# Kernel optimization log

Hardware: AMD Instinct MI355X
Metric: run time of the kernel (lower is better)

## Reference

```python
import jax, jax.numpy as jnp
import numpy as np

HEADS = 8
NEG_SLOPE = 0.2


def _gat_conv(x, src, dst, W, a_src, a_dst, b, heads, ch):
    # PyG GATConv (v1), eval mode (dropout inactive), add_self_loops=True, concat=True.
    N = x.shape[0]
    loop = jnp.arange(N)
    s = jnp.concatenate([src, loop])
    d = jnp.concatenate([dst, loop])
    h = (x @ W).reshape(N, heads, ch)                      # [N, H, C]
    alpha_src = jnp.einsum('nhc,hc->nh', h, a_src)          # [N, H]
    alpha_dst = jnp.einsum('nhc,hc->nh', h, a_dst)
    e = jax.nn.leaky_relu(alpha_src[s] + alpha_dst[d], NEG_SLOPE)  # [E, H]
    m = jax.ops.segment_max(e, d, num_segments=N)           # segment softmax over dst
    ex = jnp.exp(e - m[d])
    denom = jax.ops.segment_sum(ex, d, num_segments=N)
    alpha = ex / (denom[d] + 1e-16)
    out = jax.ops.segment_sum(h[s] * alpha[:, :, None], d, num_segments=N)  # [N, H, C]
    return out.reshape(N, heads * ch) + b


def setup_inputs() -> dict:
    key = jax.random.key(0)
    ks = jax.random.split(key, 20)
    B, N, F_in = 8, 1024, 16
    E = 131072
    C1, C2 = 8, 128                     # per-head channels of conv1 / conv2
    D = N * HEADS * C2                  # flattened head input = 1024*1024
    NA, AC = 4, 4                       # len(num_actions)=4, each 4 actions

    def w(k, shape, fan_in):
        return jax.random.normal(k, shape, jnp.float32) * (1.0 / np.sqrt(fan_in))

    inp = {
        'x': jax.random.normal(ks[0], (B, N, F_in), jnp.float32),
        'edge': jax.random.randint(ks[1], (2, E), 0, B * N, jnp.int64),
        'W1': w(ks[2], (F_in, HEADS * C1), F_in),
        'a_src1': w(ks[3], (HEADS, C1), C1),
        'a_dst1': w(ks[4], (HEADS, C1), C1),
        'b1': jnp.zeros((HEADS * C1,), jnp.float32),
        'W2': w(ks[5], (HEADS * C1, HEADS * C2), HEADS * C1),
        'a_src2': w(ks[6], (HEADS, C2), C2),
        'a_dst2': w(ks[7], (HEADS, C2), C2),
        'b2': jnp.zeros((HEADS * C2,), jnp.float32),
        'adv_w': w(ks[8], (D, NA * AC), D),
        'adv_b': jnp.zeros((NA * AC,), jnp.float32),
        'val1_w': w(ks[9], (D, 64), D),
        'val1_b': jnp.zeros((64,), jnp.float32),
        'val2_w': w(ks[10], (64, 64), 64),
        'val2_b': jnp.zeros((64,), jnp.float32),
        'val3_w': w(ks[11], (64, 1), 64),
        'val3_b': jnp.zeros((1,), jnp.float32),
    }
    return inp


def reference(x, edge, W1, a_src1, a_dst1, b1, W2, a_src2, a_dst2, b2,
              adv_w, adv_b, val1_w, val1_b, val2_w, val2_b, val3_w, val3_b):
    B, N, F_in = x.shape
    src, dst = edge[0], edge[1]
    h = x.reshape(B * N, F_in)
    h = jax.nn.relu(_gat_conv(h, src, dst, W1, a_src1, a_dst1, b1, HEADS, 8))
    h = jax.nn.relu(_gat_conv(h, src, dst, W2, a_src2, a_dst2, b2, HEADS, 128))
    h = h.reshape(B, -1)                                   # [B, N*1024]
    adv = jax.nn.relu(h @ adv_w + adv_b).reshape(B, 4, 4)  # [B, len(num_actions), actions]
    v = jax.nn.relu(h @ val1_w + val1_b)
    v = jax.nn.relu(v @ val2_w + val2_b)
    v = v @ val3_w + val3_b                                # [B, 1]
    return v[:, :, None] + adv - adv.mean(-1, keepdims=True)
```

## Files before the change

### kernel.cpp

```cpp
#include <hip/hip_runtime.h>
#include <stdint.h>

#define NODES   8192
#define BATCH   8
#define FIN     16
#define HC1     64
#define HC2     1024
#define DTOT    1048576
#define NEG     0.2f

typedef unsigned short u16;

__device__ __forceinline__ float b2f(u16 s){ return __uint_as_float(((unsigned)s)<<16); }
__device__ __forceinline__ u16 f2b(float f){
    unsigned u = __float_as_uint(f);
    unsigned r = u + 0x7fffu + ((u>>16)&1u);
    return (u16)(r>>16);
}
__device__ __forceinline__ float lrelu(float x){ return x > 0.f ? x : NEG*x; }
__device__ __forceinline__ float ldf(const void* p, long i, int isf){
    return isf ? ((const float*)p)[i] : b2f(((const u16*)p)[i]);
}

__global__ void k_detect(const u16* __restrict__ xs, const int* __restrict__ ed, int* flags){
    __shared__ int cnt[2];
    int t = threadIdx.x;
    if(t<2) cnt[t]=0;
    __syncthreads();
    int bad=0;
    for(int i=t;i<1024;i+=256){
        u16 u = xs[i];
        float a = fabsf(b2f(u));
        if(!(u==0 || (a>1e-8f && a<1e4f))) bad++;
    }
    if(bad) atomicAdd(&cnt[0], bad);
    int z=0;
    for(int i=t;i<1024;i+=256){
        if(ed[2*i+1]==0) z++;
    }
    if(z) atomicAdd(&cnt[1], z);
    __syncthreads();
    if(t==0){ flags[0] = (cnt[0] > 64) ? 1 : 0; flags[1] = (cnt[1] > 512) ? 1 : 0; }
}

__device__ __forceinline__ int esrc(const int* e, int i, int i64){ return i64 ? e[2*i] : e[i]; }
__device__ __forceinline__ int edst(const int* e, int i, int E, int i64){ return i64 ? e[2*(E+i)] : e[E+i]; }

__global__ void k_zero(int* counts){
    int i = blockIdx.x*256 + threadIdx.x;
    if(i < NODES) counts[i] = 0;
}

__global__ void k_count(const int* __restrict__ ed, int E, int* counts, const int* flags){
    int i64 = flags[1];
    int e = blockIdx.x*256 + threadIdx.x;
    if(e < E) atomicAdd(&counts[edst(ed,e,E,i64)], 1);
}

__global__ __launch_bounds__(1024) void k_scan(const int* __restrict__ counts, int* offs, int* cursor){
    __shared__ int sums[1024];
    int t = threadIdx.x;
    int base = t*8;
    int loc[8]; int s = 0;
    for(int k=0;k<8;k++){ loc[k] = s; s += counts[base+k]; }
    sums[t] = s;
    __syncthreads();
    for(int off=1; off<1024; off<<=1){
        int v = (t>=off) ? sums[t-off] : 0;
        __syncthreads();
        sums[t] += v;
        __syncthreads();
    }
    int b = (t==0) ? 0 : sums[t-1];
    for(int k=0;k<8;k++){ int v = b + loc[k]; offs[base+k]=v; cursor[base+k]=v; }
    if(t==1023) offs[NODES] = sums[1023];
}

__global__ void k_fill(const int* __restrict__ ed, int E, int* cursor, int* csr, const int* flags){
    int i64 = flags[1];
    int e = blockIdx.x*256 + threadIdx.x;
    if(e < E){ int p = atomicAdd(&cursor[edst(ed,e,E,i64)], 1); csr[p] = esrc(ed,e,i64); }
}

__global__ __launch_bounds__(256) void k_dense1(const void* __restrict__ x,
        const void* __restrict__ W1, const void* __restrict__ asw, const void* __restrict__ adw,
        float* g1, float* as1, float* ad1, const int* flags){
    int isf = flags[0];
    __shared__ float w1[FIN*HC1];
    __shared__ float av[64], dv[64];
    __shared__ float xr[4][FIN];
    __shared__ float hrow[4][HC1];
    int t = threadIdx.x;
    int n0 = blockIdx.x*4;
    for(int i=t;i<FIN*HC1;i+=256) w1[i] = ldf(W1,i,isf);
    if(t<64){ av[t]=ldf(asw,t,isf); dv[t]=ldf(adw,t,isf); }
    if(t<64) xr[t>>4][t&15] = ldf(x, n0*FIN + t, isf);
    __syncthreads();
    int i = t>>6, c = t&63;
    float acc = 0.f;
    #pragma unroll
    for(int k=0;k<FIN;k++) acc += xr[i][k]*w1[k*HC1+c];
    g1[(n0+i)*HC1 + c] = acc;
    hrow[i][c] = acc;
    __syncthreads();
    if(t<32){
        int ii=t>>3, h=t&7;
        float sa=0.f, sd=0.f;
        #pragma unroll
        for(int k=0;k<8;k++){ float v=hrow[ii][h*8+k]; sa+=v*av[h*8+k]; sd+=v*dv[h*8+k]; }
        as1[(n0+ii)*8+h]=sa; ad1[(n0+ii)*8+h]=sd;
    }
}

__global__ __launch_bounds__(64) void k_agg1(const int* __restrict__ offs, const int* __restrict__ csr,
        const float* __restrict__ g1, const float* __restrict__ as1, const float* __restrict__ ad1,
        const void* __restrict__ b1, float* z1, const int* flags){
    int isf = flags[0];
    __shared__ float redm[64], redd[64];
    __shared__ float mh[8], dh[8], adl[8];
    __shared__ int src_l[64];
    __shared__ float wx[64*8];
    int n = blockIdx.x, t = threadIdx.x;
    int off = offs[n], deg = offs[n+1]-off, tot = deg+1;
    if(t<8) adl[t] = ad1[n*8+t];
    __syncthreads();
    {
        int h = t&7, jg = t>>3;
        float ad = adl[h];
        float m = -1e30f, d = 0.f;
        for(int j=jg; j<tot; j+=8){
            int s = (j<deg)?csr[off+j]:n;
            float e = lrelu(as1[s*8+h] + ad);
            if(e>m){ d = d*__expf(m-e) + 1.f; m = e; } else d += __expf(e-m);
        }
        redm[t]=m; redd[t]=d;
        __syncthreads();
        for(int st=4; st>=1; st>>=1){
            if(jg < st){
                float m2 = redm[t + st*8], d2 = redd[t + st*8];
                float mm = fmaxf(m, m2);
                d = d*__expf(m-mm) + d2*__expf(m2-mm);
                m = mm;
                redm[t]=m; redd[t]=d;
            }
            __syncthreads();
        }
        if(t<8){ mh[t]=redm[t]; dh[t]=redd[t] + 1e-16f; }
        __syncthreads();
    }
    int c = t, hc = t>>3;
    float acc = 0.f;
    for(int c0=0;c0<tot;c0+=64){
        int nc = min(64, tot-c0);
        if(t<nc){ int j=c0+t; src_l[t]=(j<deg)?csr[off+j]:n; }
        __syncthreads();
        for(int p=t;p<nc*8;p+=64){
            int j=p>>3, hh=p&7;
            float e = lrelu(as1[src_l[j]*8+hh] + adl[hh]);
            wx[p] = __expf(e - mh[hh]);
        }
        __syncthreads();
        for(int j=0;j<nc;j++) acc += wx[j*8+hc]*g1[src_l[j]*HC1 + c];
        __syncthreads();
    }
    z1[n*HC1 + c] = fmaxf(acc/dh[hc] + ldf(b1,c,isf), 0.f);
}

__global__ __launch_bounds__(256) void k_dense2(const float* __restrict__ z1,
        const void* __restrict__ W2, u16* g2, const int* flags){
    int isf = flags[0];
    __shared__ float zr[8][HC1];
    int t = threadIdx.x;
    int n0 = blockIdx.x*8;
    for(int i=t;i<8*HC1;i+=256) zr[i>>6][i&63] = z1[n0*HC1 + i];
    __syncthreads();
    int c0 = t*4;
    float acc[8][4];
    #pragma unroll
    for(int i=0;i<8;i++){ acc[i][0]=0;acc[i][1]=0;acc[i][2]=0;acc[i][3]=0; }
    for(int k=0;k<HC1;k++){
        float w0,w1,w2,w3;
        if(isf){
            float4 w = *(const float4*)((const float*)W2 + (size_t)k*HC2 + c0);
            w0=w.x; w1=w.y; w2=w.z; w3=w.w;
        } else {
            ushort4 w = *(const ushort4*)((const u16*)W2 + (size_t)k*HC2 + c0);
            w0=b2f(w.x); w1=b2f(w.y); w2=b2f(w.z); w3=b2f(w.w);
        }
        #pragma unroll
        for(int i=0;i<8;i++){
            float zv = zr[i][k];
            acc[i][0]+=zv*w0; acc[i][1]+=zv*w1; acc[i][2]+=zv*w2; acc[i][3]+=zv*w3;
        }
    }
    #pragma unroll
    for(int i=0;i<8;i++){
        ushort4 o;
        o.x=f2b(acc[i][0]); o.y=f2b(acc[i][1]); o.z=f2b(acc[i][2]); o.w=f2b(acc[i][3]);
        *(ushort4*)&g2[(size_t)(n0+i)*HC2 + c0] = o;
    }
}

__global__ __launch_bounds__(256) void k_alpha2(const u16* __restrict__ g2,
        const void* __restrict__ asw, const void* __restrict__ adw,
        float* as2, float* ad2, const int* flags){
    int isf = flags[0];
    int n = blockIdx.x, t = threadIdx.x;
    int h = t>>5, l = t&31;
    int c = h*128 + l*4;
    ushort4 gv = *(const ushort4*)&g2[(size_t)n*HC2 + c];
    float s0,s1,s2,s3,d0,d1,d2,d3;
    if(isf){
        float4 sv = *(const float4*)((const float*)asw + c);
        float4 dv = *(const float4*)((const float*)adw + c);
        s0=sv.x;s1=sv.y;s2=sv.z;s3=sv.w; d0=dv.x;d1=dv.y;d2=dv.z;d3=dv.w;
    } else {
        ushort4 sv = *(const ushort4*)((const u16*)asw + c);
        ushort4 dv = *(const ushort4*)((const u16*)adw + c);
        s0=b2f(sv.x);s1=b2f(sv.y);s2=b2f(sv.z);s3=b2f(sv.w);
        d0=b2f(dv.x);d1=b2f(dv.y);d2=b2f(dv.z);d3=b2f(dv.w);
    }
    float g0=b2f(gv.x), g1v=b2f(gv.y), g2v=b2f(gv.z), g3=b2f(gv.w);
    float sa = g0*s0+g1v*s1+g2v*s2+g3*s3;
    float sd = g0*d0+g1v*d1+g2v*d2+g3*d3;
    for(int m=1;m<32;m<<=1){ sa += __shfl_xor(sa,m); sd += __shfl_xor(sd,m); }
    if(l==0){ as2[n*8+h]=sa; ad2[n*8+h]=sd; }
}

__global__ __launch_bounds__(256) void k_agg2(const int* __restrict__ offs, const int* __restrict__ csr,
        const u16* __restrict__ g2, const float* __restrict__ as2, const float* __restrict__ ad2,
        const void* __restrict__ b2, u16* hbf, const int* flags){
    int isf = flags[0];
    __shared__ float redm[256], redd[256];
    __shared__ float mh[8], dh[8], adl[8];
    __shared__ int src_l[64];
    __shared__ float wx[64*8];
    int n = blockIdx.x, t = threadIdx.x;
    int off = offs[n], deg = offs[n+1]-off, tot = deg+1;
    if(t<8) adl[t] = ad2[n*8+t];
    __syncthreads();
    {
        int h = t&7, jg = t>>3;
        float ad = adl[h];
        float m = -1e30f, d = 0.f;
        for(int j=jg; j<tot; j+=32){
            int s = (j<deg)?csr[off+j]:n;
            float e = lrelu(as2[s*8+h] + ad);
            if(e>m){ d = d*__expf(m-e) + 1.f; m = e; } else d += __expf(e-m);
        }
        redm[t]=m; redd[t]=d;
        __syncthreads();
        for(int st=16; st>=1; st>>=1){
            if(jg < st){
                float m2 = redm[t + st*8], d2 = redd[t + st*8];
                float mm = fmaxf(m, m2);
                d = d*__expf(m-mm) + d2*__expf(m2-mm);
                m = mm;
                redm[t]=m; redd[t]=d;
            }
            __syncthreads();
        }
        if(t<8){ mh[t]=redm[t]; dh[t]=redd[t] + 1e-16f; }
        __syncthreads();
    }
    int c0 = t*4, hc = t>>5;
    float acc[4] = {0,0,0,0};
    for(int cc0=0;cc0<tot;cc0+=64){
        int nc = min(64, tot-cc0);
        if(t<nc){ int j=cc0+t; src_l[t]=(j<deg)?csr[off+j]:n; }
        __syncthreads();
        for(int p=t;p<nc*8;p+=256){
            int j=p>>3, hh=p&7;
            float e = lrelu(as2[src_l[j]*8+hh] + adl[hh]);
            wx[p] = __expf(e - mh[hh]);
        }
        __syncthreads();
        for(int j=0;j<nc;j++){
            float w = wx[j*8+hc];
            ushort4 gv = *(const ushort4*)&g2[(size_t)src_l[j]*HC2 + c0];
            acc[0]+=w*b2f(gv.x); acc[1]+=w*b2f(gv.y); acc[2]+=w*b2f(gv.z); acc[3]+=w*b2f(gv.w);
        }
        __syncthreads();
    }
    float dhv = dh[hc];
    ushort4 o;
    o.x = f2b(fmaxf(acc[0]/dhv + ldf(b2,c0+0,isf), 0.f));
    o.y = f2b(fmaxf(acc[1]/dhv + ldf(b2,c0+1,isf), 0.f));
    o.z = f2b(fmaxf(acc[2]/dhv + ldf(b2,c0+2,isf), 0.f));
    o.w = f2b(fmaxf(acc[3]/dhv + ldf(b2,c0+3,isf), 0.f));
    *(ushort4*)&hbf[(size_t)n*HC2 + c0] = o;
}

template<int COLS, int NW>
__device__ __forceinline__ void gemv_part(const void* __restrict__ W, const u16* __restrict__ hbf,
        float* __restrict__ scratch, int wid, int lane, int isf){
    const int GR    = COLS/8;
    const int KSTEP = 64/GR;
    const int ITERS = DTOT/(NW*KSTEP);
    int cg  = (lane % GR)*8;
    int kof = lane / GR;
    float acc[8][8];
    #pragma unroll
    for(int b=0;b<8;b++)
        #pragma unroll
        for(int c=0;c<8;c++) acc[b][c]=0.f;
    for(int it=0; it<ITERS; it++){
        int k = (it*NW + wid)*KSTEP + kof;
        float wv[8];
        if(isf){
            float4 wa = *(const float4*)((const float*)W + (size_t)k*COLS + cg);
            float4 wb = *(const float4*)((const float*)W + (size_t)k*COLS + cg + 4);
            wv[0]=wa.x;wv[1]=wa.y;wv[2]=wa.z;wv[3]=wa.w;
            wv[4]=wb.x;wv[5]=wb.y;wv[6]=wb.z;wv[7]=wb.w;
        } else {
            ushort4 wa = *(const ushort4*)((const u16*)W + (size_t)k*COLS + cg);
            ushort4 wb = *(const ushort4*)((const u16*)W + (size_t)k*COLS + cg + 4);
            wv[0]=b2f(wa.x);wv[1]=b2f(wa.y);wv[2]=b2f(wa.z);wv[3]=b2f(wa.w);
            wv[4]=b2f(wb.x);wv[5]=b2f(wb.y);wv[6]=b2f(wb.z);wv[7]=b2f(wb.w);
        }
        float hv[8];
        #pragma unroll
        for(int b=0;b<8;b++) hv[b] = b2f(hbf[(size_t)b*DTOT + k]);
        #pragma unroll
        for(int b=0;b<8;b++)
            #pragma unroll
            for(int c=0;c<8;c++) acc[b][c] += hv[b]*wv[c];
    }
    #pragma unroll
    for(int m=GR;m<64;m<<=1){
        #pragma unroll
        for(int b=0;b<8;b++)
            #pragma unroll
            for(int c=0;c<8;c++) acc[b][c] += __shfl_xor(acc[b][c], m);
    }
    int q = lane / GR;
    if(q < 8){
        float4 o0, o1;
        o0.x=acc[q][0]; o0.y=acc[q][1]; o0.z=acc[q][2]; o0.w=acc[q][3];
        o1.x=acc[q][4]; o1.y=acc[q][5]; o1.z=acc[q][6]; o1.w=acc[q][7];
        float* dst = scratch + (size_t)wid*COLS*8 + q*COLS + cg;
        *(float4*)dst       = o0;
        *(float4*)(dst + 4) = o1;
    }
}

__global__ __launch_bounds__(256) void k_heads(const void* __restrict__ v1w, const void* __restrict__ advw,
        const u16* __restrict__ hbf, float* s1, float* s2, const int* flags){
    int isf = flags[0];
    int lane = threadIdx.x & 63;
    if(blockIdx.x < 512){
        int wid = (int)((blockIdx.x*256 + threadIdx.x) >> 6);
        gemv_part<64,2048>(v1w, hbf, s1, wid, lane, isf);
    } else {
        int wid = (int)(((blockIdx.x-512)*256 + threadIdx.x) >> 6);
        gemv_part<16,512>(advw, hbf, s2, wid, lane, isf);
    }
}

__global__ __launch_bounds__(256) void k_reduce(const float* __restrict__ s1, const float* __restrict__ s2,
        float* v1a, float* adva){
    __shared__ float red[256];
    int blk = blockIdx.x, t = threadIdx.x;
    if(blk < 8){
        int o = blk*64 + (t&63);
        float a = 0.f;
        for(int p = (t>>6); p < 2048; p += 4) a += s1[(size_t)p*512 + o];
        red[t] = a; __syncthreads();
        if(t<64) v1a[o] = red[t]+red[t+64]+red[t+128]+red[t+192];
    } else {
        int o = (blk-8)*64 + (t&63);
        float a = 0.f;
        for(int p = (t>>6); p < 512; p += 4) a += s2[(size_t)p*128 + o];
        red[t] = a; __syncthreads();
        if(t<64) adva[o] = red[t]+red[t+64]+red[t+128]+red[t+192];
    }
}

__global__ __launch_bounds__(512) void k_final(const float* __restrict__ v1a, const float* __restrict__ adva,
        const void* __restrict__ v1b, const void* __restrict__ advb,
        const void* __restrict__ w2v, const void* __restrict__ b2v,
        const void* __restrict__ w3v, const void* __restrict__ b3v,
        void* out, const int* flags){
    int isf = flags[0];
    __shared__ float v1[8][64], v2[8][64], adv[128], v3[8];
    int t = threadIdx.x;
    { int b=t>>6, j=t&63; v1[b][j] = fmaxf(v1a[t] + ldf(v1b,j,isf), 0.f); }
    if(t<128) adv[t] = fmaxf(adva[t] + ldf(advb,t&15,isf), 0.f);
    __syncthreads();
    { int b=t>>6, j=t&63;
      float a=0.f;
      for(int k=0;k<64;k++) a += v1[b][k]*ldf(w2v,k*64+j,isf);
      v2[b][j] = fmaxf(a + ldf(b2v,j,isf), 0.f); }
    __syncthreads();
    if(t<8){
        float a=0.f;
        for(int k=0;k<64;k++) a += v2[t][k]*ldf(w3v,k,isf);
        v3[t] = a + ldf(b3v,0,isf);
    }
    __syncthreads();
    if(t<128){
        int b=t>>4, r=(t>>2)&3;
        int base = b*16 + r*4;
        float m = 0.25f*(adv[base]+adv[base+1]+adv[base+2]+adv[base+3]);
        float val = v3[b] + adv[t] - m;
        if(isf) ((float*)out)[t] = val;
        else    ((u16*)out)[t]   = f2b(val);
    }
}

extern "C" void kernel_launch(void* const* d_in, const int* in_sizes, int n_in,
                              void* d_out, int out_size, void* d_ws, size_t ws_size,
                              hipStream_t stream){
    const void* x    = d_in[0];
    const int*  edge = (const int*)d_in[1];
    const int E = in_sizes[1]/2;
    const void* W1   = d_in[2];
    const void* as1w = d_in[3];
    const void* ad1w = d_in[4];
    const void* b1   = d_in[5];
    const void* W2   = d_in[6];
    const void* as2w = d_in[7];
    const void* ad2w = d_in[8];
    const void* b2   = d_in[9];
    const void* advw = d_in[10];
    const void* advb = d_in[11];
    const void* v1w  = d_in[12];
    const void* v1b  = d_in[13];
    const void* v2w  = d_in[14];
    const void* v2b  = d_in[15];
    const void* v3w  = d_in[16];
    const void* v3b  = d_in[17];

    char* wsp = (char*)d_ws;
    size_t o = 0;
    auto alloc = [&](size_t bytes)->char*{
        char* p = wsp + o;
        o = (o + bytes + 255) & ~(size_t)255;
        return p;
    };
    int*   flags  = (int*)  alloc(256);
    int*   counts = (int*)  alloc(NODES*4);
    int*   offs   = (int*)  alloc((NODES+8)*4);
    int*   cursor = (int*)  alloc(NODES*4);
    int*   csr    = (int*)  alloc((size_t)E*4);
    float* g1     = (float*)alloc((size_t)NODES*HC1*4);
    float* as1    = (float*)alloc((size_t)NODES*8*4);
    float* ad1    = (float*)alloc((size_t)NODES*8*4);
    float* z1     = (float*)alloc((size_t)NODES*HC1*4);
    u16*   g2     = (u16*)  alloc((size_t)NODES*HC2*2);
    float* as2    = (float*)alloc((size_t)NODES*8*4);
    float* ad2    = (float*)alloc((size_t)NODES*8*4);
    u16*   hbf    = (u16*)  alloc((size_t)NODES*HC2*2);
    float* s1     = (float*)alloc((size_t)2048*512*4);
    float* s2     = (float*)alloc((size_t)512*128*4);
    float* v1a    = (float*)alloc(512*4);
    float* adva   = (float*)alloc(128*4);

    k_detect<<<1, 256, 0, stream>>>((const u16*)x, edge, flags);
    k_zero  <<<32, 256, 0, stream>>>(counts);
    k_count <<<(E+255)/256, 256, 0, stream>>>(edge, E, counts, flags);
    k_scan  <<<1, 1024, 0, stream>>>(counts, offs, cursor);
    k_fill  <<<(E+255)/256, 256, 0, stream>>>(edge, E, cursor, csr, flags);
    k_dense1<<<NODES/4, 256, 0, stream>>>(x, W1, as1w, ad1w, g1, as1, ad1, flags);
    k_agg1  <<<NODES, 64, 0, stream>>>(offs, csr, g1, as1, ad1, b1, z1, flags);
    k_dense2<<<NODES/8, 256, 0, stream>>>(z1, W2, g2, flags);
    k_alpha2<<<NODES, 256, 0, stream>>>(g2, as2w, ad2w, as2, ad2, flags);
    k_agg2  <<<NODES, 256, 0, stream>>>(offs, csr, g2, as2, ad2, b2, hbf, flags);
    k_heads <<<640, 256, 0, stream>>>(v1w, advw, hbf, s1, s2, flags);
    k_reduce<<<10, 256, 0, stream>>>(s1, s2, v1a, adva);
    k_final <<<1, 512, 0, stream>>>(v1a, adva, v1b, advb, v2w, v2b, v3w, v3b, d_out, flags);
}
```

Baseline: 720.6 us.

## Fuse prep/count/dense1 and dense2/alpha2 kernels, unroll gathers, widen head GEMV grid

Merges flag detection with counter zeroing, edge counting with the first dense layer, and the second dense layer with its attention-logit computation, cutting kernel launches and a full re-read of g2. The neighbor-gather loops in both aggregation kernels are unrolled by two to expose more memory-level parallelism. The head GEMV doubles its block count with two k-steps per iteration, and the partial-sum reduction moves to 1024-thread blocks. The larger partial buffers add reduction traffic, and the alpha2 logits are now computed from fp32 accumulators instead of bf16-rounded values, which slightly changes numerics.

```diff
diff --git a/kernel.cpp b/kernel.cpp
--- a/kernel.cpp
+++ b/kernel.cpp
@@ -22,39 +22,71 @@
     return isf ? ((const float*)p)[i] : b2f(((const u16*)p)[i]);
 }
 
-__global__ void k_detect(const u16* __restrict__ xs, const int* __restrict__ ed, int* flags){
-    __shared__ int cnt[2];
-    int t = threadIdx.x;
-    if(t<2) cnt[t]=0;
-    __syncthreads();
-    int bad=0;
-    for(int i=t;i<1024;i+=256){
-        u16 u = xs[i];
-        float a = fabsf(b2f(u));
-        if(!(u==0 || (a>1e-8f && a<1e4f))) bad++;
-    }
-    if(bad) atomicAdd(&cnt[0], bad);
-    int z=0;
-    for(int i=t;i<1024;i+=256){
-        if(ed[2*i+1]==0) z++;
-    }
-    if(z) atomicAdd(&cnt[1], z);
-    __syncthreads();
-    if(t==0){ flags[0] = (cnt[0] > 64) ? 1 : 0; flags[1] = (cnt[1] > 512) ? 1 : 0; }
-}
-
 __device__ __forceinline__ int esrc(const int* e, int i, int i64){ return i64 ? e[2*i] : e[i]; }
 __device__ __forceinline__ int edst(const int* e, int i, int E, int i64){ return i64 ? e[2*(E+i)] : e[E+i]; }
 
-__global__ void k_zero(int* counts){
-    int i = blockIdx.x*256 + threadIdx.x;
-    if(i < NODES) counts[i] = 0;
-}
-
-__global__ void k_count(const int* __restrict__ ed, int E, int* counts, const int* flags){
-    int i64 = flags[1];
-    int e = blockIdx.x*256 + threadIdx.x;
-    if(e < E) atomicAdd(&counts[edst(ed,e,E,i64)], 1);
+__global__ __launch_bounds__(256) void k_prep(const u16* __restrict__ xs, const int* __restrict__ ed,
+        int* flags, int* counts){
+    int t = threadIdx.x;
+    if(blockIdx.x == 0){
+        __shared__ int cnt[2];
+        if(t<2) cnt[t]=0;
+        __syncthreads();
+        int bad=0;
+        for(int i=t;i<1024;i+=256){
+            u16 u = xs[i];
+            float a = fabsf(b2f(u));
+            if(!(u==0 || (a>1e-8f && a<1e4f))) bad++;
+        }
+        if(bad) atomicAdd(&cnt[0], bad);
+        int z=0;
+        for(int i=t;i<1024;i+=256){
+            if(ed[2*i+1]==0) z++;
+        }
+        if(z) atomicAdd(&cnt[1], z);
+        __syncthreads();
+        if(t==0){ flags[0] = (cnt[0] > 64) ? 1 : 0; flags[1] = (cnt[1] > 512) ? 1 : 0; }
+    } else {
+        int i = (blockIdx.x-1)*256 + t;
+        if(i < NODES) counts[i] = 0;
+    }
+}
+
+__global__ __launch_bounds__(256) void k_cnt_d1(const int* __restrict__ ed, int E, int* counts,
+        const void* __restrict__ x, const void* __restrict__ W1,
+        const void* __restrict__ asw, const void* __restrict__ adw,
+        float* g1, float* as1, float* ad1, const int* flags){
+    int t = threadIdx.x;
+    if(blockIdx.x < 512){
+        int i64 = flags[1];
+        int e = blockIdx.x*256 + t;
+        if(e < E) atomicAdd(&counts[edst(ed,e,E,i64)], 1);
+        return;
+    }
+    int isf = flags[0];
+    __shared__ float w1[FIN*HC1];
+    __shared__ float av[64], dv[64];
+    __shared__ float xr[4][FIN];
+    __shared__ float hrow[4][HC1];
+    int n0 = (blockIdx.x-512)*4;
+    for(int i=t;i<FIN*HC1;i+=256) w1[i] = ldf(W1,i,isf);
+    if(t<64){ av[t]=ldf(asw,t,isf); dv[t]=ldf(adw,t,isf); }
+    if(t<64) xr[t>>4][t&15] = ldf(x, n0*FIN + t, isf);
+    __syncthreads();
+    int i = t>>6, c = t&63;
+    float acc = 0.f;
+    #pragma unroll
+    for(int k=0;k<FIN;k++) acc += xr[i][k]*w1[k*HC1+c];
+    g1[(n0+i)*HC1 + c] = acc;
+    hrow[i][c] = acc;
+    __syncthreads();
+    if(t<32){
+        int ii=t>>3, h=t&7;
+        float sa=0.f, sd=0.f;
+        #pragma unroll
+        for(int k=0;k<8;k++){ float v=hrow[ii][h*8+k]; sa+=v*av[h*8+k]; sd+=v*dv[h*8+k]; }
+        as1[(n0+ii)*8+h]=sa; ad1[(n0+ii)*8+h]=sd;
+    }
 }
 
 __global__ __launch_bounds__(1024) void k_scan(const int* __restrict__ counts, int* offs, int* cursor){
@@ -80,36 +112,6 @@
     int i64 = flags[1];
     int e = blockIdx.x*256 + threadIdx.x;
     if(e < E){ int p = atomicAdd(&cursor[edst(ed,e,E,i64)], 1); csr[p] = esrc(ed,e,i64); }
-}
-
-__global__ __launch_bounds__(256) void k_dense1(const void* __restrict__ x,
-        const void* __restrict__ W1, const void* __restrict__ asw, const void* __restrict__ adw,
-        float* g1, float* as1, float* ad1, const int* flags){
-    int isf = flags[0];
-    __shared__ float w1[FIN*HC1];
-    __shared__ float av[64], dv[64];
-    __shared__ float xr[4][FIN];
-    __shared__ float hrow[4][HC1];
-    int t = threadIdx.x;
-    int n0 = blockIdx.x*4;
-    for(int i=t;i<FIN*HC1;i+=256) w1[i] = ldf(W1,i,isf);
-    if(t<64){ av[t]=ldf(asw,t,isf); dv[t]=ldf(adw,t,isf); }
-    if(t<64) xr[t>>4][t&15] = ldf(x, n0*FIN + t, isf);
-    __syncthreads();
-    int i = t>>6, c = t&63;
-    float acc = 0.f;
-    #pragma unroll
-    for(int k=0;k<FIN;k++) acc += xr[i][k]*w1[k*HC1+c];
-    g1[(n0+i)*HC1 + c] = acc;
-    hrow[i][c] = acc;
-    __syncthreads();
-    if(t<32){
-        int ii=t>>3, h=t&7;
-        float sa=0.f, sd=0.f;
-        #pragma unroll
-        for(int k=0;k<8;k++){ float v=hrow[ii][h*8+k]; sa+=v*av[h*8+k]; sd+=v*dv[h*8+k]; }
-        as1[(n0+ii)*8+h]=sa; ad1[(n0+ii)*8+h]=sd;
-    }
 }
 
 __global__ __launch_bounds__(64) void k_agg1(const int* __restrict__ offs, const int* __restrict__ csr,
@@ -160,19 +162,28 @@
             wx[p] = __expf(e - mh[hh]);
         }
         __syncthreads();
-        for(int j=0;j<nc;j++) acc += wx[j*8+hc]*g1[src_l[j]*HC1 + c];
+        int j = 0;
+        for(; j+2<=nc; j+=2){
+            float w0 = wx[j*8+hc],     v0 = g1[src_l[j]*HC1 + c];
+            float w1 = wx[(j+1)*8+hc], v1 = g1[src_l[j+1]*HC1 + c];
+            acc += w0*v0 + w1*v1;
+        }
+        if(j<nc) acc += wx[j*8+hc]*g1[src_l[j]*HC1 + c];
         __syncthreads();
     }
     z1[n*HC1 + c] = fmaxf(acc/dh[hc] + ldf(b1,c,isf), 0.f);
 }
 
-__global__ __launch_bounds__(256) void k_dense2(const float* __restrict__ z1,
-        const void* __restrict__ W2, u16* g2, const int* flags){
+__global__ __launch_bounds__(256) void k_d2a2(const float* __restrict__ z1,
+        const void* __restrict__ W2, const void* __restrict__ asw, const void* __restrict__ adw,
+        u16* g2, float* as2, float* ad2, const int* flags){
     int isf = flags[0];
     __shared__ float zr[8][HC1];
+    __shared__ float avs[HC2], ads[HC2];
     int t = threadIdx.x;
     int n0 = blockIdx.x*8;
     for(int i=t;i<8*HC1;i+=256) zr[i>>6][i&63] = z1[n0*HC1 + i];
+    for(int i=t;i<HC2;i+=256){ avs[i]=ldf(asw,i,isf); ads[i]=ldf(adw,i,isf); }
     __syncthreads();
     int c0 = t*4;
     float acc[8][4];
@@ -193,38 +204,20 @@
             acc[i][0]+=zv*w0; acc[i][1]+=zv*w1; acc[i][2]+=zv*w2; acc[i][3]+=zv*w3;
         }
     }
+    float a0=avs[c0], a1=avs[c0+1], a2=avs[c0+2], a3=avs[c0+3];
+    float d0=ads[c0], d1=ads[c0+1], d2=ads[c0+2], d3=ads[c0+3];
+    int h = t>>5;
     #pragma unroll
     for(int i=0;i<8;i++){
         ushort4 o;
         o.x=f2b(acc[i][0]); o.y=f2b(acc[i][1]); o.z=f2b(acc[i][2]); o.w=f2b(acc[i][3]);
         *(ushort4*)&g2[(size_t)(n0+i)*HC2 + c0] = o;
-    }
-}
-
-__global__ __launch_bounds__(256) void k_alpha2(const u16* __restrict__ g2,
-        const void* __restrict__ asw, const void* __restrict__ adw,
-        float* as2, float* ad2, const int* flags){
-    int isf = flags[0];
-    int n = blockIdx.x, t = threadIdx.x;
-    int h = t>>5, l = t&31;
-    int c = h*128 + l*4;
-    ushort4 gv = *(const ushort4*)&g2[(size_t)n*HC2 + c];
-    float s0,s1,s2,s3,d0,d1,d2,d3;
-    if(isf){
-        float4 sv = *(const float4*)((const float*)asw + c);
-        float4 dv = *(const float4*)((const float*)adw + c);
-        s0=sv.x;s1=sv.y;s2=sv.z;s3=sv.w; d0=dv.x;d1=dv.y;d2=dv.z;d3=dv.w;
-    } else {
-        ushort4 sv = *(const ushort4*)((const u16*)asw + c);
-        ushort4 dv = *(const ushort4*)((const u16*)adw + c);
-        s0=b2f(sv.x);s1=b2f(sv.y);s2=b2f(sv.z);s3=b2f(sv.w);
-        d0=b2f(dv.x);d1=b2f(dv.y);d2=b2f(dv.z);d3=b2f(dv.w);
-    }
-    float g0=b2f(gv.x), g1v=b2f(gv.y), g2v=b2f(gv.z), g3=b2f(gv.w);
-    float sa = g0*s0+g1v*s1+g2v*s2+g3*s3;
-    float sd = g0*d0+g1v*d1+g2v*d2+g3*d3;
-    for(int m=1;m<32;m<<=1){ sa += __shfl_xor(sa,m); sd += __shfl_xor(sd,m); }
-    if(l==0){ as2[n*8+h]=sa; ad2[n*8+h]=sd; }
+        float pa = acc[i][0]*a0 + acc[i][1]*a1 + acc[i][2]*a2 + acc[i][3]*a3;
+        float pd = acc[i][0]*d0 + acc[i][1]*d1 + acc[i][2]*d2 + acc[i][3]*d3;
+        #pragma unroll
+        for(int m=1;m<32;m<<=1){ pa += __shfl_xor(pa,m); pd += __shfl_xor(pd,m); }
+        if((t&31)==0){ as2[(n0+i)*8+h]=pa; ad2[(n0+i)*8+h]=pd; }
+    }
 }
 
 __global__ __launch_bounds__(256) void k_agg2(const int* __restrict__ offs, const int* __restrict__ csr,
@@ -275,7 +268,17 @@
             wx[p] = __expf(e - mh[hh]);
         }
         __syncthreads();
-        for(int j=0;j<nc;j++){
+        int j = 0;
+        for(; j+2<=nc; j+=2){
+            float w0 = wx[j*8+hc], w1 = wx[(j+1)*8+hc];
+            ushort4 gv0 = *(const ushort4*)&g2[(size_t)src_l[j]*HC2 + c0];
+            ushort4 gv1 = *(const ushort4*)&g2[(size_t)src_l[j+1]*HC2 + c0];
+            acc[0]+=w0*b2f(gv0.x)+w1*b2f(gv1.x);
+            acc[1]+=w0*b2f(gv0.y)+w1*b2f(gv1.y);
+            acc[2]+=w0*b2f(gv0.z)+w1*b2f(gv1.z);
+            acc[3]+=w0*b2f(gv0.w)+w1*b2f(gv1.w);
+        }
+        if(j<nc){
             float w = wx[j*8+hc];
             ushort4 gv = *(const ushort4*)&g2[(size_t)src_l[j]*HC2 + c0];
             acc[0]+=w*b2f(gv.x); acc[1]+=w*b2f(gv.y); acc[2]+=w*b2f(gv.z); acc[3]+=w*b2f(gv.w);
@@ -304,27 +307,34 @@
     for(int b=0;b<8;b++)
         #pragma unroll
         for(int c=0;c<8;c++) acc[b][c]=0.f;
-    for(int it=0; it<ITERS; it++){
-        int k = (it*NW + wid)*KSTEP + kof;
-        float wv[8];
+    for(int it=0; it<ITERS; it+=2){
+        int k0 = (it*NW + wid)*KSTEP + kof;
+        int k1 = ((it+1)*NW + wid)*KSTEP + kof;
+        float wv0[8], wv1[8];
         if(isf){
-            float4 wa = *(const float4*)((const float*)W + (size_t)k*COLS + cg);
-            float4 wb = *(const float4*)((const float*)W + (size_t)k*COLS + cg + 4);
-            wv[0]=wa.x;wv[1]=wa.y;wv[2]=wa.z;wv[3]=wa.w;
-            wv[4]=wb.x;wv[5]=wb.y;wv[6]=wb.z;wv[7]=wb.w;
+            float4 a0 = *(const float4*)((const float*)W + (size_t)k0*COLS + cg);
+            float4 b0 = *(const float4*)((const float*)W + (size_t)k0*COLS + cg + 4);
+            float4 a1 = *(const float4*)((const float*)W + (size_t)k1*COLS + cg);
+            float4 b1 = *(const float4*)((const float*)W + (size_t)k1*COLS + cg + 4);
+            wv0[0]=a0.x;wv0[1]=a0.y;wv0[2]=a0.z;wv0[3]=a0.w;wv0[4]=b0.x;wv0[5]=b0.y;wv0[6]=b0.z;wv0[7]=b0.w;
+            wv1[0]=a1.x;wv1[1]=a1.y;wv1[2]=a1.z;wv1[3]=a1.w;wv1[4]=b1.x;wv1[5]=b1.y;wv1[6]=b1.z;wv1[7]=b1.w;
         } else {
-            ushort4 wa = *(const ushort4*)((const u16*)W + (size_t)k*COLS + cg);
-            ushort4 wb = *(const ushort4*)((const u16*)W + (size_t)k*COLS + cg + 4);
-            wv[0]=b2f(wa.x);wv[1]=b2f(wa.y);wv[2]=b2f(wa.z);wv[3]=b2f(wa.w);
-            wv[4]=b2f(wb.x);wv[5]=b2f(wb.y);wv[6]=b2f(wb.z);wv[7]=b2f(wb.w);
-        }
-        float hv[8];
-        #pragma unroll
-        for(int b=0;b<8;b++) hv[b] = b2f(hbf[(size_t)b*DTOT + k]);
+            ushort4 a0 = *(const ushort4*)((const u16*)W + (size_t)k0*COLS + cg);
+            ushort4 b0 = *(const ushort4*)((const u16*)W + (size_t)k0*COLS + cg + 4);
+            ushort4 a1 = *(const ushort4*)((const u16*)W + (size_t)k1*COLS + cg);
+            ushort4 b1 = *(const ushort4*)((const u16*)W + (size_t)k1*COLS + cg + 4);
+            wv0[0]=b2f(a0.x);wv0[1]=b2f(a0.y);wv0[2]=b2f(a0.z);wv0[3]=b2f(a0.w);
+            wv0[4]=b2f(b0.x);wv0[5]=b2f(b0.y);wv0[6]=b2f(b0.z);wv0[7]=b2f(b0.w);
+            wv1[0]=b2f(a1.x);wv1[1]=b2f(a1.y);wv1[2]=b2f(a1.z);wv1[3]=b2f(a1.w);
+            wv1[4]=b2f(b1.x);wv1[5]=b2f(b1.y);wv1[6]=b2f(b1.z);wv1[7]=b2f(b1.w);
+        }
+        float hv0[8], hv1[8];
+        #pragma unroll
+        for(int b=0;b<8;b++){ hv0[b] = b2f(hbf[(size_t)b*DTOT + k0]); hv1[b] = b2f(hbf[(size_t)b*DTOT + k1]); }
         #pragma unroll
         for(int b=0;b<8;b++)
             #pragma unroll
-            for(int c=0;c<8;c++) acc[b][c] += hv[b]*wv[c];
+            for(int c=0;c<8;c++) acc[b][c] += hv0[b]*wv0[c] + hv1[b]*wv1[c];
     }
     #pragma unroll
     for(int m=GR;m<64;m<<=1){
@@ -348,31 +358,31 @@
         const u16* __restrict__ hbf, float* s1, float* s2, const int* flags){
     int isf = flags[0];
     int lane = threadIdx.x & 63;
-    if(blockIdx.x < 512){
+    if(blockIdx.x < 1024){
         int wid = (int)((blockIdx.x*256 + threadIdx.x) >> 6);
-        gemv_part<64,2048>(v1w, hbf, s1, wid, lane, isf);
+        gemv_part<64,4096>(v1w, hbf, s1, wid, lane, isf);
     } else {
-        int wid = (int)(((blockIdx.x-512)*256 + threadIdx.x) >> 6);
-        gemv_part<16,512>(advw, hbf, s2, wid, lane, isf);
-    }
-}
-
-__global__ __launch_bounds__(256) void k_reduce(const float* __restrict__ s1, const float* __restrict__ s2,
+        int wid = (int)(((blockIdx.x-1024)*256 + threadIdx.x) >> 6);
+        gemv_part<16,1024>(advw, hbf, s2, wid, lane, isf);
+    }
+}
+
+__global__ __launch_bounds__(1024) void k_reduce(const float* __restrict__ s1, const float* __restrict__ s2,
         float* v1a, float* adva){
-    __shared__ float red[256];
+    __shared__ float red[1024];
     int blk = blockIdx.x, t = threadIdx.x;
+    int ph = t>>6, ln = t&63;
+    float a = 0.f;
     if(blk < 8){
-        int o = blk*64 + (t&63);
-        float a = 0.f;
-        for(int p = (t>>6); p < 2048; p += 4) a += s1[(size_t)p*512 + o];
+        int o = blk*64 + ln;
+        for(int p = ph; p < 4096; p += 16) a += s1[(size_t)p*512 + o];
         red[t] = a; __syncthreads();
-        if(t<64) v1a[o] = red[t]+red[t+64]+red[t+128]+red[t+192];
+        if(t<64){ float s=0.f; for(int q=0;q<16;q++) s += red[q*64+t]; v1a[blk*64+t]=s; }
     } else {
-        int o = (blk-8)*64 + (t&63);
-        float a = 0.f;
-        for(int p = (t>>6); p < 512; p += 4) a += s2[(size_t)p*128 + o];
+        int o = (blk-8)*64 + ln;
+        for(int p = ph; p < 1024; p += 16) a += s2[(size_t)p*128 + o];
         red[t] = a; __syncthreads();
-        if(t<64) adva[o] = red[t]+red[t+64]+red[t+128]+red[t+192];
+        if(t<64){ float s=0.f; for(int q=0;q<16;q++) s += red[q*64+t]; adva[(blk-8)*64+t]=s; }
     }
 }
 
@@ -451,22 +461,19 @@
     float* as2    = (float*)alloc((size_t)NODES*8*4);
     float* ad2    = (float*)alloc((size_t)NODES*8*4);
     u16*   hbf    = (u16*)  alloc((size_t)NODES*HC2*2);
-    float* s1     = (float*)alloc((size_t)2048*512*4);
-    float* s2     = (float*)alloc((size_t)512*128*4);
+    float* s1     = (float*)alloc((size_t)4096*512*4);
+    float* s2     = (float*)alloc((size_t)1024*128*4);
     float* v1a    = (float*)alloc(512*4);
     float* adva   = (float*)alloc(128*4);
 
-    k_detect<<<1, 256, 0, stream>>>((const u16*)x, edge, flags);
-    k_zero  <<<32, 256, 0, stream>>>(counts);
-    k_count <<<(E+255)/256, 256, 0, stream>>>(edge, E, counts, flags);
+    k_prep  <<<33, 256, 0, stream>>>((const u16*)x, edge, flags, counts);
+    k_cnt_d1<<<2560, 256, 0, stream>>>(edge, E, counts, x, W1, as1w, ad1w, g1, as1, ad1, flags);
     k_scan  <<<1, 1024, 0, stream>>>(counts, offs, cursor);
     k_fill  <<<(E+255)/256, 256, 0, stream>>>(edge, E, cursor, csr, flags);
-    k_dense1<<<NODES/4, 256, 0, stream>>>(x, W1, as1w, ad1w, g1, as1, ad1, flags);
     k_agg1  <<<NODES, 64, 0, stream>>>(offs, csr, g1, as1, ad1, b1, z1, flags);
-    k_dense2<<<NODES/8, 256, 0, stream>>>(z1, W2, g2, flags);
-    k_alpha2<<<NODES, 256, 0, stream>>>(g2, as2w, ad2w, as2, ad2, flags);
+    k_d2a2  <<<NODES/8, 256, 0, stream>>>(z1, W2, as2w, ad2w, g2, as2, ad2, flags);
     k_agg2  <<<NODES, 256, 0, stream>>>(offs, csr, g2, as2, ad2, b2, hbf, flags);
-    k_heads <<<640, 256, 0, stream>>>(v1w, advw, hbf, s1, s2, flags);
-    k_reduce<<<10, 256, 0, stream>>>(s1, s2, v1a, adva);
+    k_heads <<<1280, 256, 0, stream>>>(v1w, advw, hbf, s1, s2, flags);
+    k_reduce<<<10, 1024, 0, stream>>>(s1, s2, v1a, adva);
     k_final <<<1, 512, 0, stream>>>(v1a, adva, v1b, advb, v2w, v2b, v3w, v3b, d_out, flags);
 }
```

Result: faster. 681.4 us (-5.4%).
